# Kernel tuning notes

Hardware: AMD Instinct MI355X
Metric: run time of the kernel (lower is better)

Reference implementation:

```python
import jax, jax.numpy as jnp
import numpy as np

N = 100000
E = 1600000
HID = 128
NODE_DIM = 128


def _sage_conv(h, src, dst, W_l, b_l, W_r, n_nodes):
    # PyG SAGEConv (mean aggr): out = lin_l(mean_{j in N(i)} h_j) + lin_r(h_i)
    msg = h[src]                                            # [E, d] gather
    s = jax.ops.segment_sum(msg, dst, num_segments=n_nodes)  # [N, d]
    cnt = jax.ops.segment_sum(jnp.ones((msg.shape[0], 1), h.dtype), dst,
                              num_segments=n_nodes)          # [N, 1]
    agg = jnp.where(cnt > 0, s / jnp.maximum(cnt, 1.0), 0.0)
    return agg @ W_l + b_l + h @ W_r


def setup_inputs() -> dict:
    key = jax.random.key(0)
    ks = jax.random.split(key, 12)
    sc = 0.05
    return {
        "pos": jax.random.normal(ks[0], (N, 3), jnp.float32),
        "atomic_number": jax.random.randint(ks[1], (N,), 0, 10, jnp.int64)
            if jax.config.jax_enable_x64 else jax.random.randint(ks[1], (N,), 0, 10, jnp.int32),
        "edge_index": jax.random.randint(ks[2], (2, E), 0, N, jnp.int32),
        # input_proj: Linear(4, HID) — stored as [in, out]
        "W_in": jax.random.normal(ks[3], (4, HID), jnp.float32) * sc,
        "b_in": jnp.zeros((HID,), jnp.float32),
        # conv1: SAGEConv(HID, HID): lin_l (bias), lin_r (no bias)
        "W1_l": jax.random.normal(ks[4], (HID, HID), jnp.float32) * sc,
        "b1": jnp.zeros((HID,), jnp.float32),
        "W1_r": jax.random.normal(ks[5], (HID, HID), jnp.float32) * sc,
        # conv2
        "W2_l": jax.random.normal(ks[6], (HID, HID), jnp.float32) * sc,
        "b2": jnp.zeros((HID,), jnp.float32),
        "W2_r": jax.random.normal(ks[7], (HID, HID), jnp.float32) * sc,
        # out: Linear(HID, NODE_DIM)
        "W_out": jax.random.normal(ks[8], (HID, NODE_DIM), jnp.float32) * sc,
        "b_out": jnp.zeros((NODE_DIM,), jnp.float32),
    }


def reference(pos, atomic_number, edge_index, W_in, b_in, W1_l, b1, W1_r,
              W2_l, b2, W2_r, W_out, b_out):
    src, dst = edge_index[0], edge_index[1]
    z_atom = (atomic_number.astype(pos.dtype) / 10.0)[:, None]   # [N, 1]
    x = jnp.concatenate([z_atom, pos], axis=-1)                   # [N, 4]
    h = jax.nn.relu(x @ W_in + b_in)
    h = jax.nn.relu(_sage_conv(h, src, dst, W1_l, b1, W1_r, h.shape[0]))
    h = jax.nn.relu(_sage_conv(h, src, dst, W2_l, b2, W2_r, h.shape[0]))
    node_states = h @ W_out + b_out                               # [N, node_dim]
    return node_states.mean(axis=0), node_states
```

## Files before the change

### kernel.cpp

```cpp
#include <hip/hip_runtime.h>

#define HID 128
#define BK_SHIFT 9
#define BK_NODES 512
#define BKCAP 10240
#define EDGES_PER_BLKA 8192

typedef _Float16 half_t;
typedef __attribute__((ext_vector_type(8))) _Float16 half8;
typedef __attribute__((ext_vector_type(4))) _Float16 half4;
typedef __attribute__((ext_vector_type(4))) float f32x4;

__global__ __launch_bounds__(256) void k_setup(const float* __restrict__ pos,
                                               const int* __restrict__ an,
                                               const float* __restrict__ Win,
                                               const float* __restrict__ bin,
                                               half_t* __restrict__ h0,
                                               const float* __restrict__ w0,
                                               const float* __restrict__ w1,
                                               const float* __restrict__ w2,
                                               const float* __restrict__ w3,
                                               const float* __restrict__ w4,
                                               half_t* __restrict__ o0,
                                               half_t* __restrict__ o1,
                                               half_t* __restrict__ o2,
                                               half_t* __restrict__ o3,
                                               half_t* __restrict__ o4,
                                               int* __restrict__ bcur,
                                               float* __restrict__ outmean,
                                               half_t* __restrict__ h0z,
                                               half_t* __restrict__ h1z,
                                               int n, int gEmbed) {
  int bid = blockIdx.x;
  if (bid < gEmbed) {
    int t = bid * 256 + threadIdx.x;
    int i = t >> 5, cg = t & 31;
    if (i >= n) return;
    int j0 = cg << 2;
    float z  = (float)an[i] / 10.0f;
    float px = pos[3 * i + 0], py = pos[3 * i + 1], pz = pos[3 * i + 2];
    float4 ww0 = *(const float4*)&Win[0 * HID + j0];
    float4 ww1 = *(const float4*)&Win[1 * HID + j0];
    float4 ww2 = *(const float4*)&Win[2 * HID + j0];
    float4 ww3 = *(const float4*)&Win[3 * HID + j0];
    float4 b   = *(const float4*)&bin[j0];
    float4 o;
    o.x = fmaxf(fmaf(z, ww0.x, fmaf(px, ww1.x, fmaf(py, ww2.x, fmaf(pz, ww3.x, b.x)))), 0.f);
    o.y = fmaxf(fmaf(z, ww0.y, fmaf(px, ww1.y, fmaf(py, ww2.y, fmaf(pz, ww3.y, b.y)))), 0.f);
    o.z = fmaxf(fmaf(z, ww0.z, fmaf(px, ww1.z, fmaf(py, ww2.z, fmaf(pz, ww3.z, b.z)))), 0.f);
    o.w = fmaxf(fmaf(z, ww0.w, fmaf(px, ww1.w, fmaf(py, ww2.w, fmaf(pz, ww3.w, b.w)))), 0.f);
    half4 ph;
    ph.x = (half_t)o.x; ph.y = (half_t)o.y; ph.z = (half_t)o.z; ph.w = (half_t)o.w;
    *(half4*)&h0[(size_t)i * HID + j0] = ph;
  } else if (bid < gEmbed + 40) {
    int pb = bid - gEmbed;
    int m = pb >> 3;
    const float* W = (m == 0) ? w0 : (m == 1) ? w1 : (m == 2) ? w2 : (m == 3) ? w3 : w4;
    half_t* out = (m == 0) ? o0 : (m == 1) ? o1 : (m == 2) ? o2 : (m == 3) ? o3 : o4;
    int tid = (pb & 7) * 256 + threadIdx.x;
    int lane = tid & 63;
    int frag = tid >> 6;
    int ks = frag >> 3, nt = frag & 7;
    int k0 = ks * 32 + ((lane >> 4) << 3);
    int col = nt * 16 + (lane & 15);
    half8 v;
#pragma unroll
    for (int i = 0; i < 8; ++i) v[i] = (half_t)W[(k0 + i) * HID + col];
    *(half8*)&out[(size_t)tid * 8] = v;
  } else {
    int i = threadIdx.x;
    bcur[i] = i * BKCAP;
    if (i < HID) outmean[i] = 0.f;
    if (i < HID) h0z[i] = (half_t)0.f;
    else         h1z[i - HID] = (half_t)0.f;
  }
}

__global__ __launch_bounds__(1024) void k_bucketA(const int* __restrict__ src,
                                                  const int* __restrict__ dst,
                                                  int* __restrict__ bcur,
                                                  unsigned* __restrict__ ebuf,
                                                  int e) {
  __shared__ int hist[256];
  __shared__ int resv[256];
  int t = threadIdx.x;
  if (t < 256) hist[t] = 0;
  __syncthreads();
  int base = blockIdx.x * EDGES_PER_BLKA + t * 8;
  int myb[8], myr[8];
  unsigned mypk[8];
  if (base + 8 <= e) {
    int4 sa = *(const int4*)&src[base];
    int4 sb = *(const int4*)&src[base + 4];
    int4 da = *(const int4*)&dst[base];
    int4 db = *(const int4*)&dst[base + 4];
    int ss[8] = {sa.x, sa.y, sa.z, sa.w, sb.x, sb.y, sb.z, sb.w};
    int dd[8] = {da.x, da.y, da.z, da.w, db.x, db.y, db.z, db.w};
#pragma unroll
    for (int i = 0; i < 8; ++i) {
      int b = dd[i] >> BK_SHIFT;
      myb[i] = b;
      myr[i] = atomicAdd(&hist[b], 1);
      mypk[i] = ((unsigned)ss[i] << BK_SHIFT) | (unsigned)(dd[i] & (BK_NODES - 1));
    }
  } else {
#pragma unroll
    for (int i = 0; i < 8; ++i) {
      int idx = base + i;
      if (idx < e) {
        int d = dst[idx];
        int s = src[idx];
        int b = d >> BK_SHIFT;
        myb[i] = b;
        myr[i] = atomicAdd(&hist[b], 1);
        mypk[i] = ((unsigned)s << BK_SHIFT) | (unsigned)(d & (BK_NODES - 1));
      } else {
        myb[i] = -1;
      }
    }
  }
  __syncthreads();
  if (t < 256) resv[t] = (hist[t] > 0) ? atomicAdd(&bcur[t], hist[t]) : 0;
  __syncthreads();
#pragma unroll
  for (int i = 0; i < 8; ++i) {
    if (myb[i] >= 0) ebuf[resv[myb[i]] + myr[i]] = mypk[i];
  }
}

__global__ __launch_bounds__(512) void k_bucketB(const unsigned* __restrict__ ebuf,
                                                 const int* __restrict__ bkend,
                                                 int* __restrict__ offs,
                                                 int* __restrict__ offsE,
                                                 int* __restrict__ csr, int n) {
  __shared__ int hist[BK_NODES];
  __shared__ int red[BK_NODES];
  int b = blockIdx.x;
  int n0 = b << BK_SHIFT;
  int t = threadIdx.x;
  int ebeg = b * BKCAP, eend = bkend[b];
  hist[t] = 0;
  __syncthreads();
  for (int idx = ebeg + t * 4; idx < eend; idx += 2048) {
    if (idx + 4 <= eend) {
      uint4 pk = *(const uint4*)&ebuf[idx];
      atomicAdd(&hist[pk.x & (BK_NODES - 1)], 1);
      atomicAdd(&hist[pk.y & (BK_NODES - 1)], 1);
      atomicAdd(&hist[pk.z & (BK_NODES - 1)], 1);
      atomicAdd(&hist[pk.w & (BK_NODES - 1)], 1);
    } else {
      for (int k = 0; k < 4; ++k) {
        int id2 = idx + k;
        if (id2 < eend) atomicAdd(&hist[ebuf[id2] & (BK_NODES - 1)], 1);
      }
    }
  }
  __syncthreads();
  int h0 = hist[t];
  red[t] = h0;
  __syncthreads();
  for (int d = 1; d < 512; d <<= 1) {
    int u = (t >= d) ? red[t - d] : 0;
    __syncthreads();
    red[t] += u;
    __syncthreads();
  }
  int base0 = ebeg + (red[t] - h0);
  int g = n0 + t;
  if (g < n) { offs[g] = base0; offsE[g] = base0 + h0; }
  __syncthreads();
  hist[t] = base0;
  __syncthreads();
  for (int idx = ebeg + t * 4; idx < eend; idx += 2048) {
    if (idx + 4 <= eend) {
      uint4 pk = *(const uint4*)&ebuf[idx];
      csr[atomicAdd(&hist[pk.x & (BK_NODES - 1)], 1)] = (int)(pk.x >> BK_SHIFT);
      csr[atomicAdd(&hist[pk.y & (BK_NODES - 1)], 1)] = (int)(pk.y >> BK_SHIFT);
      csr[atomicAdd(&hist[pk.z & (BK_NODES - 1)], 1)] = (int)(pk.z >> BK_SHIFT);
      csr[atomicAdd(&hist[pk.w & (BK_NODES - 1)], 1)] = (int)(pk.w >> BK_SHIFT);
    } else {
      for (int k = 0; k < 4; ++k) {
        int id2 = idx + k;
        if (id2 < eend) {
          unsigned pk = ebuf[id2];
          csr[atomicAdd(&hist[pk & (BK_NODES - 1)], 1)] = (int)(pk >> BK_SHIFT);
        }
      }
    }
  }
}

__global__ __launch_bounds__(256) void k_aggmean_f16(const half_t* __restrict__ h,
                                                     const int* __restrict__ csr,
                                                     const int* __restrict__ offs,
                                                     const int* __restrict__ offsE,
                                                     half_t* __restrict__ out, int n) {
  int w = (blockIdx.x * 256 + threadIdx.x) >> 6;
  int lane = threadIdx.x & 63;
  if (w >= n) return;
  int cs = lane & 15, es = lane >> 4;
  int beg = offs[w], end = offsE[w];
  size_t coff = (size_t)(cs * 8);
  float acc[8];
#pragma unroll
  for (int j = 0; j < 8; ++j) acc[j] = 0.f;
  int e = beg;
  for (; e + 16 <= end; e += 16) {
    int s0 = csr[e + es];
    int s1 = csr[e + 4 + es];
    int s2 = csr[e + 8 + es];
    int s3 = csr[e + 12 + es];
    half8 v0 = *(const half8*)&h[(size_t)s0 * HID + coff];
    half8 v1 = *(const half8*)&h[(size_t)s1 * HID + coff];
    half8 v2 = *(const half8*)&h[(size_t)s2 * HID + coff];
    half8 v3 = *(const half8*)&h[(size_t)s3 * HID + coff];
#pragma unroll
    for (int j = 0; j < 8; ++j)
      acc[j] += ((float)v0[j] + (float)v1[j]) + ((float)v2[j] + (float)v3[j]);
  }
  for (; e < end; e += 4) {
    int ee = e + es;
    if (ee < end) {
      int s = csr[ee];
      half8 v = *(const half8*)&h[(size_t)s * HID + coff];
#pragma unroll
      for (int j = 0; j < 8; ++j) acc[j] += (float)v[j];
    }
  }
#pragma unroll
  for (int j = 0; j < 8; ++j) {
    acc[j] += __shfl_xor(acc[j], 16, 64);
    acc[j] += __shfl_xor(acc[j], 32, 64);
  }
  if (es == 0) {
    int c = end - beg;
    float inv = (c > 0) ? 1.0f / (float)c : 0.0f;
    half8 o;
#pragma unroll
    for (int j = 0; j < 8; ++j) o[j] = (half_t)(acc[j] * inv);
    *(half8*)&out[(size_t)w * HID + coff] = o;
  }
}

__global__ __launch_bounds__(256) void k_sage_mfma(const half_t* __restrict__ ha,
                                                   const half_t* __restrict__ hs,
                                                   const half_t* __restrict__ wl,
                                                   const half_t* __restrict__ wr,
                                                   const float* __restrict__ bias,
                                                   half_t* __restrict__ out, int n) {
  int lane = threadIdx.x & 63;
  int wid = threadIdx.x >> 6;
  int row0 = blockIdx.x * 64 + wid * 16;
  if (row0 >= n) return;
  int arow = row0 + (lane & 15);
  int arowc = arow < n ? arow : n - 1;
  size_t abase = (size_t)arowc * HID + ((lane >> 4) << 3);
  const half8* WL = (const half8*)wl;
  const half8* WR = (const half8*)wr;
  f32x4 acc[8];
#pragma unroll
  for (int t = 0; t < 8; ++t) acc[t] = (f32x4){0.f, 0.f, 0.f, 0.f};
#pragma unroll
  for (int ks = 0; ks < 4; ++ks) {
    half8 aD = *(const half8*)&ha[abase + ks * 32];
    half8 aH = *(const half8*)&hs[abase + ks * 32];
    int fb = ks * 8;
#pragma unroll
    for (int nt = 0; nt < 8; ++nt) {
      half8 bl = WL[(size_t)(fb + nt) * 64 + lane];
      half8 br = WR[(size_t)(fb + nt) * 64 + lane];
      acc[nt] = __builtin_amdgcn_mfma_f32_16x16x32_f16(aD, bl, acc[nt], 0, 0, 0);
      acc[nt] = __builtin_amdgcn_mfma_f32_16x16x32_f16(aH, br, acc[nt], 0, 0, 0);
    }
  }
  int rbase = row0 + ((lane >> 4) << 2);
  int cl = lane & 15;
#pragma unroll
  for (int nt = 0; nt < 8; ++nt) {
    int col = nt * 16 + cl;
    float bv = bias[col];
#pragma unroll
    for (int r = 0; r < 4; ++r) {
      int row = rbase + r;
      if (row < n) {
        float v = fmaxf(acc[nt][r] + bv, 0.f);
        out[(size_t)row * HID + col] = (half_t)v;
      }
    }
  }
}

__global__ __launch_bounds__(256) void k_sage_out(const half_t* __restrict__ ha,
                                                  const half_t* __restrict__ hs,
                                                  const half_t* __restrict__ wl,
                                                  const half_t* __restrict__ wr,
                                                  const float* __restrict__ bias2,
                                                  const half_t* __restrict__ wout,
                                                  const float* __restrict__ bout,
                                                  float* __restrict__ out,
                                                  float* __restrict__ part, int n) {
  __shared__ half_t Hs[64][132];
  __shared__ float colsum[HID];
  int tid = threadIdx.x;
  int lane = tid & 63;
  int wid = tid >> 6;
  if (tid < HID) colsum[tid] = 0.f;
  int row0 = blockIdx.x * 64 + wid * 16;
  bool active = row0 < n;

  if (active) {
    int arow = row0 + (lane & 15);
    int arowc = arow < n ? arow : n - 1;
    size_t abase = (size_t)arowc * HID + ((lane >> 4) << 3);
    const half8* WL = (const half8*)wl;
    const half8* WR = (const half8*)wr;
    f32x4 acc[8];
#pragma unroll
    for (int t = 0; t < 8; ++t) acc[t] = (f32x4){0.f, 0.f, 0.f, 0.f};
#pragma unroll
    for (int ks = 0; ks < 4; ++ks) {
      half8 aD = *(const half8*)&ha[abase + ks * 32];
      half8 aH = *(const half8*)&hs[abase + ks * 32];
      int fb = ks * 8;
#pragma unroll
      for (int nt = 0; nt < 8; ++nt) {
        half8 bl = WL[(size_t)(fb + nt) * 64 + lane];
        half8 br = WR[(size_t)(fb + nt) * 64 + lane];
        acc[nt] = __builtin_amdgcn_mfma_f32_16x16x32_f16(aD, bl, acc[nt], 0, 0, 0);
        acc[nt] = __builtin_amdgcn_mfma_f32_16x16x32_f16(aH, br, acc[nt], 0, 0, 0);
      }
    }
    int rb = (lane >> 4) << 2;
    int cl = lane & 15;
#pragma unroll
    for (int nt = 0; nt < 8; ++nt) {
      int col = nt * 16 + cl;
      float bv = bias2[col];
#pragma unroll
      for (int r = 0; r < 4; ++r) {
        float v = fmaxf(acc[nt][r] + bv, 0.f);
        Hs[wid * 16 + rb + r][col] = (half_t)v;
      }
    }
  }
  __syncthreads();

  if (active) {
    int lrow = wid * 16 + (lane & 15);
    int koff = (lane >> 4) << 3;
    const half8* W8 = (const half8*)wout;
    f32x4 acc2[8];
#pragma unroll
    for (int t = 0; t < 8; ++t) acc2[t] = (f32x4){0.f, 0.f, 0.f, 0.f};
#pragma unroll
    for (int ks = 0; ks < 4; ++ks) {
      half8 aH = *(const half8*)&Hs[lrow][ks * 32 + koff];
      int fb = ks * 8;
#pragma unroll
      for (int nt = 0; nt < 8; ++nt) {
        half8 b = W8[(size_t)(fb + nt) * 64 + lane];
        acc2[nt] = __builtin_amdgcn_mfma_f32_16x16x32_f16(aH, b, acc2[nt], 0, 0, 0);
      }
    }
    int rbase = row0 + ((lane >> 4) << 2);
    int cl = lane & 15;
#pragma unroll
    for (int nt = 0; nt < 8; ++nt) {
      int col = nt * 16 + cl;
      float bv = bout[col];
      float csum = 0.f;
#pragma unroll
      for (int r = 0; r < 4; ++r) {
        int row = rbase + r;
        if (row < n) {
          float v = acc2[nt][r] + bv;
          out[(size_t)row * HID + col] = v;
          csum += v;
        }
      }
      atomicAdd(&colsum[col], csum);
    }
  }
  __syncthreads();
  if (tid < HID) part[(size_t)blockIdx.x * HID + tid] = colsum[tid];
}

__global__ __launch_bounds__(256) void k_colfinal(const float* __restrict__ part,
                                                  float* __restrict__ outmean,
                                                  int rows, float inv) {
  __shared__ float red[256];
  int t = threadIdx.x;
  int col = t & 127, half = t >> 7;
  int r0 = blockIdx.x * 256;
  float s = 0.f;
  for (int r = half; r < 256; r += 2) {
    int row = r0 + r;
    if (row < rows) s += part[(size_t)row * HID + col];
  }
  red[t] = s;
  __syncthreads();
  if (t < 128) atomicAdd(&outmean[col], (red[t] + red[t + 128]) * inv);
}

extern "C" void kernel_launch(void* const* d_in, const int* in_sizes, int n_in,
                              void* d_out, int out_size, void* d_ws, size_t ws_size,
                              hipStream_t stream) {
  const float* pos  = (const float*)d_in[0];
  const int*   an   = (const int*)d_in[1];
  const int*   ei   = (const int*)d_in[2];
  const float* Win  = (const float*)d_in[3];
  const float* bin  = (const float*)d_in[4];
  const float* W1l  = (const float*)d_in[5];
  const float* b1   = (const float*)d_in[6];
  const float* W1r  = (const float*)d_in[7];
  const float* W2l  = (const float*)d_in[8];
  const float* b2   = (const float*)d_in[9];
  const float* W2r  = (const float*)d_in[10];
  const float* Wout = (const float*)d_in[11];
  const float* bout = (const float*)d_in[12];

  int N = in_sizes[0] / 3;
  int E = in_sizes[2] / 2;
  const int* srcl = ei;
  const int* dstl = ei + E;

  float* outmean = (float*)d_out;
  float* ns      = (float*)d_out + HID;

  char* p = (char*)d_ws;
  auto take = [&](size_t bytes) {
    char* q = p;
    p += (bytes + 255) & ~(size_t)255;
    return q;
  };
  int nbuck = (N + BK_NODES - 1) / BK_NODES;
  half_t*   H0      = (half_t*)take((size_t)(N + 1) * HID * 2);
  half_t*   H1      = (half_t*)take((size_t)(N + 1) * HID * 2);
  half_t*   D       = (half_t*)take((size_t)N * HID * 2);
  int*      offs    = (int*)take((size_t)N * 4);
  int*      offsE   = (int*)take((size_t)N * 4);
  int*      csr     = (int*)take((size_t)nbuck * BKCAP * 4);
  unsigned* ebuf    = (unsigned*)take((size_t)nbuck * BKCAP * 4);
  int*      bcur    = (int*)take((size_t)256 * 4);
  half_t*   pW1l    = (half_t*)take((size_t)16384 * 2);
  half_t*   pW1r    = (half_t*)take((size_t)16384 * 2);
  half_t*   pW2l    = (half_t*)take((size_t)16384 * 2);
  half_t*   pW2r    = (half_t*)take((size_t)16384 * 2);
  half_t*   pWout   = (half_t*)take((size_t)16384 * 2);
  int gSage = (N + 63) / 64;
  float*    colpart = (float*)take((size_t)gSage * HID * 4);

  int gEmbed = (int)(((size_t)N * 32 + 255) / 256);
  int gWave  = (N + 3) / 4;
  int gBktA  = (E + EDGES_PER_BLKA - 1) / EDGES_PER_BLKA;

  k_setup<<<gEmbed + 41, 256, 0, stream>>>(pos, an, Win, bin, H0,
                                           W1l, W1r, W2l, W2r, Wout,
                                           pW1l, pW1r, pW2l, pW2r, pWout,
                                           bcur, outmean,
                                           &H0[(size_t)N * HID], &H1[(size_t)N * HID],
                                           N, gEmbed);
  k_bucketA<<<gBktA, 1024, 0, stream>>>(srcl, dstl, bcur, ebuf, E);
  k_bucketB<<<nbuck, 512, 0, stream>>>(ebuf, bcur, offs, offsE, csr, N);

  k_aggmean_f16<<<gWave, 256, 0, stream>>>(H0, csr, offs, offsE, D, N);
  k_sage_mfma<<<gSage, 256, 0, stream>>>(D, H0, pW1l, pW1r, b1, H1, N);
  k_aggmean_f16<<<gWave, 256, 0, stream>>>(H1, csr, offs, offsE, D, N);
  k_sage_out<<<gSage, 256, 0, stream>>>(D, H1, pW2l, pW2r, b2, pWout, bout, ns, colpart, N);
  k_colfinal<<<(gSage + 255) / 256, 256, 0, stream>>>(colpart, outmean, gSage, 1.0f / (float)N);
}
```

Baseline: 278.3 us.

## Store node features in 16-column slabs and aggregate one slab per block

Node feature tensors are changed from row-major [N,128] to eight column slabs of [N+1,16], each row 32 bytes. The mean-aggregation kernel now runs one grid slice per slab, so each slice's gather working set (about 3.2 MB) can stay resident in cache instead of the whole 25.6 MB feature matrix. Each wave handles 32 edges at a time with 2 lanes per row, and out-of-range edges point at a zero padding row. The cost is an 8x replay of CSR index and offset reads, more shuffle reductions, and strided A-operand loads in the MFMA kernels.

```diff
diff --git a/kernel.cpp b/kernel.cpp
--- a/kernel.cpp
+++ b/kernel.cpp
@@ -5,11 +5,13 @@
 #define BK_NODES 512
 #define BKCAP 10240
 #define EDGES_PER_BLKA 8192
+#define NSLAB 8
 
 typedef _Float16 half_t;
 typedef __attribute__((ext_vector_type(8))) _Float16 half8;
 typedef __attribute__((ext_vector_type(4))) _Float16 half4;
 typedef __attribute__((ext_vector_type(4))) float f32x4;
+
 
 __global__ __launch_bounds__(256) void k_setup(const float* __restrict__ pos,
                                                const int* __restrict__ an,
@@ -28,9 +30,9 @@
                                                half_t* __restrict__ o4,
                                                int* __restrict__ bcur,
                                                float* __restrict__ outmean,
-                                               half_t* __restrict__ h0z,
-                                               half_t* __restrict__ h1z,
+                                               half_t* __restrict__ h1,
                                                int n, int gEmbed) {
+  size_t np1s = (size_t)(n + 1) * 16;
   int bid = blockIdx.x;
   if (bid < gEmbed) {
     int t = bid * 256 + threadIdx.x;
@@ -51,7 +53,7 @@
     o.w = fmaxf(fmaf(z, ww0.w, fmaf(px, ww1.w, fmaf(py, ww2.w, fmaf(pz, ww3.w, b.w)))), 0.f);
     half4 ph;
     ph.x = (half_t)o.x; ph.y = (half_t)o.y; ph.z = (half_t)o.z; ph.w = (half_t)o.w;
-    *(half4*)&h0[(size_t)i * HID + j0] = ph;
+    *(half4*)&h0[(size_t)(j0 >> 4) * np1s + (size_t)i * 16 + (j0 & 15)] = ph;
   } else if (bid < gEmbed + 40) {
     int pb = bid - gEmbed;
     int m = pb >> 3;
@@ -71,8 +73,11 @@
     int i = threadIdx.x;
     bcur[i] = i * BKCAP;
     if (i < HID) outmean[i] = 0.f;
-    if (i < HID) h0z[i] = (half_t)0.f;
-    else         h1z[i - HID] = (half_t)0.f;
+    if (i < HID) {
+      int slab = i >> 4, colin = i & 15;
+      h0[(size_t)slab * np1s + (size_t)n * 16 + colin] = (half_t)0.f;
+      h1[(size_t)slab * np1s + (size_t)n * 16 + colin] = (half_t)0.f;
+    }
   }
 }
 
@@ -190,45 +195,41 @@
   }
 }
 
-__global__ __launch_bounds__(256) void k_aggmean_f16(const half_t* __restrict__ h,
-                                                     const int* __restrict__ csr,
-                                                     const int* __restrict__ offs,
-                                                     const int* __restrict__ offsE,
-                                                     half_t* __restrict__ out, int n) {
-  int w = (blockIdx.x * 256 + threadIdx.x) >> 6;
+__global__ __launch_bounds__(256) void k_aggmean_sl(const half_t* __restrict__ h,
+                                                    const int* __restrict__ csr,
+                                                    const int* __restrict__ offs,
+                                                    const int* __restrict__ offsE,
+                                                    half_t* __restrict__ out,
+                                                    int n, int gNode) {
+  int bid = blockIdx.x;
+  int slice = bid / gNode;
+  int nblk = bid - slice * gNode;
+  int wid = threadIdx.x >> 6;
   int lane = threadIdx.x & 63;
+  int w = nblk * 4 + wid;
   if (w >= n) return;
-  int cs = lane & 15, es = lane >> 4;
+  int es = lane >> 1, cs = lane & 1;
+  size_t slab = (size_t)slice * (size_t)(n + 1) * 16;
+  const half_t* hs = h + slab;
   int beg = offs[w], end = offsE[w];
-  size_t coff = (size_t)(cs * 8);
   float acc[8];
 #pragma unroll
   for (int j = 0; j < 8; ++j) acc[j] = 0.f;
-  int e = beg;
-  for (; e + 16 <= end; e += 16) {
-    int s0 = csr[e + es];
-    int s1 = csr[e + 4 + es];
-    int s2 = csr[e + 8 + es];
-    int s3 = csr[e + 12 + es];
-    half8 v0 = *(const half8*)&h[(size_t)s0 * HID + coff];
-    half8 v1 = *(const half8*)&h[(size_t)s1 * HID + coff];
-    half8 v2 = *(const half8*)&h[(size_t)s2 * HID + coff];
-    half8 v3 = *(const half8*)&h[(size_t)s3 * HID + coff];
-#pragma unroll
-    for (int j = 0; j < 8; ++j)
-      acc[j] += ((float)v0[j] + (float)v1[j]) + ((float)v2[j] + (float)v3[j]);
-  }
-  for (; e < end; e += 4) {
-    int ee = e + es;
-    if (ee < end) {
-      int s = csr[ee];
-      half8 v = *(const half8*)&h[(size_t)s * HID + coff];
-#pragma unroll
-      for (int j = 0; j < 8; ++j) acc[j] += (float)v[j];
-    }
+  int last = end - 1;
+  for (int e = beg; e < end; e += 32) {
+    int idx = e + es;
+    int cidx = idx <= last ? idx : last;
+    int sr = csr[cidx];
+    int row = (idx <= last) ? sr : n;
+    half8 v = *(const half8*)&hs[(size_t)row * 16 + cs * 8];
+#pragma unroll
+    for (int j = 0; j < 8; ++j) acc[j] += (float)v[j];
   }
 #pragma unroll
   for (int j = 0; j < 8; ++j) {
+    acc[j] += __shfl_xor(acc[j], 2, 64);
+    acc[j] += __shfl_xor(acc[j], 4, 64);
+    acc[j] += __shfl_xor(acc[j], 8, 64);
     acc[j] += __shfl_xor(acc[j], 16, 64);
     acc[j] += __shfl_xor(acc[j], 32, 64);
   }
@@ -238,7 +239,7 @@
     half8 o;
 #pragma unroll
     for (int j = 0; j < 8; ++j) o[j] = (half_t)(acc[j] * inv);
-    *(half8*)&out[(size_t)w * HID + coff] = o;
+    *(half8*)&out[slab + (size_t)w * 16 + cs * 8] = o;
   }
 }
 
@@ -248,13 +249,14 @@
                                                    const half_t* __restrict__ wr,
                                                    const float* __restrict__ bias,
                                                    half_t* __restrict__ out, int n) {
+  size_t np1s = (size_t)(n + 1) * 16;
   int lane = threadIdx.x & 63;
   int wid = threadIdx.x >> 6;
   int row0 = blockIdx.x * 64 + wid * 16;
   if (row0 >= n) return;
   int arow = row0 + (lane & 15);
   int arowc = arow < n ? arow : n - 1;
-  size_t abase = (size_t)arowc * HID + ((lane >> 4) << 3);
+  int koff = (lane >> 4) << 3;
   const half8* WL = (const half8*)wl;
   const half8* WR = (const half8*)wr;
   f32x4 acc[8];
@@ -262,8 +264,10 @@
   for (int t = 0; t < 8; ++t) acc[t] = (f32x4){0.f, 0.f, 0.f, 0.f};
 #pragma unroll
   for (int ks = 0; ks < 4; ++ks) {
-    half8 aD = *(const half8*)&ha[abase + ks * 32];
-    half8 aH = *(const half8*)&hs[abase + ks * 32];
+    int col0 = ks * 32 + koff;
+    size_t adr = (size_t)(col0 >> 4) * np1s + (size_t)arowc * 16 + (col0 & 15);
+    half8 aD = *(const half8*)&ha[adr];
+    half8 aH = *(const half8*)&hs[adr];
     int fb = ks * 8;
 #pragma unroll
     for (int nt = 0; nt < 8; ++nt) {
@@ -284,7 +288,7 @@
       int row = rbase + r;
       if (row < n) {
         float v = fmaxf(acc[nt][r] + bv, 0.f);
-        out[(size_t)row * HID + col] = (half_t)v;
+        out[(size_t)nt * np1s + (size_t)row * 16 + cl] = (half_t)v;
       }
     }
   }
@@ -301,6 +305,7 @@
                                                   float* __restrict__ part, int n) {
   __shared__ half_t Hs[64][132];
   __shared__ float colsum[HID];
+  size_t np1s = (size_t)(n + 1) * 16;
   int tid = threadIdx.x;
   int lane = tid & 63;
   int wid = tid >> 6;
@@ -311,7 +316,7 @@
   if (active) {
     int arow = row0 + (lane & 15);
     int arowc = arow < n ? arow : n - 1;
-    size_t abase = (size_t)arowc * HID + ((lane >> 4) << 3);
+    int koff = (lane >> 4) << 3;
     const half8* WL = (const half8*)wl;
     const half8* WR = (const half8*)wr;
     f32x4 acc[8];
@@ -319,8 +324,10 @@
     for (int t = 0; t < 8; ++t) acc[t] = (f32x4){0.f, 0.f, 0.f, 0.f};
 #pragma unroll
     for (int ks = 0; ks < 4; ++ks) {
-      half8 aD = *(const half8*)&ha[abase + ks * 32];
-      half8 aH = *(const half8*)&hs[abase + ks * 32];
+      int col0 = ks * 32 + koff;
+      size_t adr = (size_t)(col0 >> 4) * np1s + (size_t)arowc * 16 + (col0 & 15);
+      half8 aD = *(const half8*)&ha[adr];
+      half8 aH = *(const half8*)&hs[adr];
       int fb = ks * 8;
 #pragma unroll
       for (int nt = 0; nt < 8; ++nt) {
@@ -434,9 +441,10 @@
     return q;
   };
   int nbuck = (N + BK_NODES - 1) / BK_NODES;
-  half_t*   H0      = (half_t*)take((size_t)(N + 1) * HID * 2);
-  half_t*   H1      = (half_t*)take((size_t)(N + 1) * HID * 2);
-  half_t*   D       = (half_t*)take((size_t)N * HID * 2);
+  size_t tsz = (size_t)NSLAB * (N + 1) * 16 * 2;
+  half_t*   H0      = (half_t*)take(tsz);
+  half_t*   H1      = (half_t*)take(tsz);
+  half_t*   D       = (half_t*)take(tsz);
   int*      offs    = (int*)take((size_t)N * 4);
   int*      offsE   = (int*)take((size_t)N * 4);
   int*      csr     = (int*)take((size_t)nbuck * BKCAP * 4);
@@ -451,21 +459,21 @@
   float*    colpart = (float*)take((size_t)gSage * HID * 4);
 
   int gEmbed = (int)(((size_t)N * 32 + 255) / 256);
-  int gWave  = (N + 3) / 4;
+  int gNode  = (N + 3) / 4;
+  int gAgg   = NSLAB * gNode;
   int gBktA  = (E + EDGES_PER_BLKA - 1) / EDGES_PER_BLKA;
 
   k_setup<<<gEmbed + 41, 256, 0, stream>>>(pos, an, Win, bin, H0,
                                            W1l, W1r, W2l, W2r, Wout,
                                            pW1l, pW1r, pW2l, pW2r, pWout,
-                                           bcur, outmean,
-                                           &H0[(size_t)N * HID], &H1[(size_t)N * HID],
+                                           bcur, outmean, H1,
                                            N, gEmbed);
   k_bucketA<<<gBktA, 1024, 0, stream>>>(srcl, dstl, bcur, ebuf, E);
   k_bucketB<<<nbuck, 512, 0, stream>>>(ebuf, bcur, offs, offsE, csr, N);
 
-  k_aggmean_f16<<<gWave, 256, 0, stream>>>(H0, csr, offs, offsE, D, N);
+  k_aggmean_sl<<<gAgg, 256, 0, stream>>>(H0, csr, offs, offsE, D, N, gNode);
   k_sage_mfma<<<gSage, 256, 0, stream>>>(D, H0, pW1l, pW1r, b1, H1, N);
-  k_aggmean_f16<<<gWave, 256, 0, stream>>>(H1, csr, offs, offsE, D, N);
+  k_aggmean_sl<<<gAgg, 256, 0, stream>>>(H1, csr, offs, offsE, D, N, gNode);
   k_sage_out<<<gSage, 256, 0, stream>>>(D, H1, pW2l, pW2r, b2, pWout, bout, ns, colpart, N);
   k_colfinal<<<(gSage + 255) / 256, 256, 0, stream>>>(colpart, outmean, gSage, 1.0f / (float)N);
 }
```

Measured after the change: 802.0 us. +188.2%, slower.
